# Optimization experiments

Hardware: AMD Instinct MI355X
Metric: run time of the kernel (lower is better)

The kernel has to match this reference:

```python
import jax, jax.numpy as jnp
import numpy as np


def _apply_ry(state, theta, i, n):
    # state: [B, 2^n] complex; theta: scalar or [B]
    B = state.shape[0]
    s = state.reshape(B, 2**i, 2, 2**(n - i - 1))
    th = jnp.reshape(theta, (-1, 1, 1)) * 0.5
    c, sn = jnp.cos(th), jnp.sin(th)
    a0, a1 = s[:, :, 0], s[:, :, 1]
    return jnp.stack([c * a0 - sn * a1, sn * a0 + c * a1], axis=2).reshape(B, -1)


def _apply_rz(state, theta, i, n):
    B = state.shape[0]
    s = state.reshape(B, 2**i, 2, 2**(n - i - 1))
    ph = jnp.exp(-0.5j * jnp.reshape(theta, (-1, 1, 1)).astype(jnp.float32))
    return jnp.stack([s[:, :, 0] * ph, s[:, :, 1] * jnp.conj(ph)], axis=2).reshape(B, -1)


def _apply_cnot(state, c, t, n):
    # CNOT(control=c, target=t); flips target amplitudes on control=1 slice
    B = state.shape[0]
    s = state.reshape((B,) + (2,) * n)
    ax_c, ax_t = 1 + c, 1 + t
    zero = jnp.take(s, 0, axis=ax_c)
    one = jnp.take(s, 1, axis=ax_c)
    one = jnp.flip(one, axis=ax_t - (1 if t > c else 0))
    return jnp.stack([zero, one], axis=ax_c).reshape(B, -1)


def _z_signs(n):
    # signs[i, k] = +1 if bit i of basis index k is 0 else -1 (qubit 0 = MSB)
    idx = np.arange(2**n)
    bits = (idx[None, :] >> (n - 1 - np.arange(n))[:, None]) & 1
    return jnp.asarray(1.0 - 2.0 * bits, dtype=jnp.float32)  # [n, 2^n]


def _circuit(q_in, w_ry, w_rz):
    # Batched state-vector simulation of: AngleEmbedding(RY) ->
    # n_layers x (per-qubit RY,RZ + CNOT ring) -> <Z_i> expectations.
    B, n = q_in.shape
    L = w_ry.shape[0]
    state = jnp.zeros((B, 2**n), jnp.complex64).at[:, 0].set(1.0)
    for i in range(n):  # AngleEmbedding with rotation='Y'
        state = _apply_ry(state, q_in[:, i], i, n)
    for l in range(L):
        for i in range(n):
            state = _apply_ry(state, w_ry[l, i], i, n)
            state = _apply_rz(state, w_rz[l, i], i, n)
        for i in range(n):  # CNOT ring
            state = _apply_cnot(state, i, (i + 1) % n, n)
    probs = jnp.abs(state) ** 2  # [B, 2^n]
    return probs @ _z_signs(n).T  # [B, n] = <Z_i>


def setup_inputs():
    key = jax.random.key(0)
    ks = jax.random.split(key, 6)
    B, D, n, L = 4096, 512, 10, 4
    return {
        "x": jax.random.normal(ks[0], (B, D), jnp.float32),
        "pre_w": jax.random.normal(ks[1], (n, D), jnp.float32) / np.sqrt(D).astype(np.float32),
        "pre_b": jnp.zeros((n,), jnp.float32),
        "post_w": jax.random.normal(ks[2], (1, n), jnp.float32) / np.sqrt(n).astype(np.float32),
        "post_b": jnp.zeros((1,), jnp.float32),
        "w_ry": jax.random.normal(ks[3], (L, n), jnp.float32),
        "w_rz": jax.random.normal(ks[4], (L, n), jnp.float32),
    }


def reference(x, pre_w, pre_b, post_w, post_b, w_ry, w_rz):
    q_in = x @ pre_w.T + pre_b      # pre_net: [B, n_qubits] rotation angles
    z = _circuit(q_in, w_ry, w_rz)  # [B, n_qubits] PauliZ expectations
    return z @ post_w.T + post_b    # post_net: [B, 1] logits
```

## Files before the change

### kernel.cpp

```cpp
#include <hip/hip_runtime.h>

#define DEV static __device__ __forceinline__

template <int CTRL>
DEV float dpp_mov(float v) {
    int i = __float_as_int(v);
    i = __builtin_amdgcn_update_dpp(i, i, CTRL, 0xF, 0xF, false);
    return __int_as_float(i);
}
template <int PAT>
DEV float swz(float v) {
    return __int_as_float(__builtin_amdgcn_ds_swizzle(__float_as_int(v), PAT));
}
DEV float bperm(int byteaddr, float v) {
    return __int_as_float(__builtin_amdgcn_ds_bpermute(byteaddr, __float_as_int(v)));
}

#if __has_builtin(__builtin_amdgcn_permlane16_swap)
#define HAVE_PL16 1
DEV void pl16_pair(float v, float &r0, float &r1) {
    auto r = __builtin_amdgcn_permlane16_swap(__float_as_int(v), __float_as_int(v),
                                              false, false);
    r0 = __int_as_float((int)r[0]);
    r1 = __int_as_float((int)r[1]);
}
#endif
#if __has_builtin(__builtin_amdgcn_permlane32_swap)
#define HAVE_PL32 1
DEV void pl32_pair(float v, float &r0, float &r1) {
    auto r = __builtin_amdgcn_permlane32_swap(__float_as_int(v), __float_as_int(v),
                                              false, false);
    r0 = __int_as_float((int)r[0]);
    r1 = __int_as_float((int)r[1]);
}
#endif

DEV float wave_sum(float v, int a32) {
    v += dpp_mov<0xB1>(v);
    v += dpp_mov<0x4E>(v);
    v += dpp_mov<0x141>(v);
    v += dpp_mov<0x128>(v);
#ifdef HAVE_PL16
    {
        float r0, r1;
        pl16_pair(v, r0, r1);
        v = r0 + r1;
    }
#else
    v += swz<0x401F>(v);
#endif
#ifdef HAVE_PL32
    {
        float r0, r1;
        pl32_pair(v, r0, r1);
        v = r0 + r1;
    }
#else
    v += bperm(a32, v);
#endif
    return v;
}

template <int P>
DEV void apply_ry(float (&re)[16], float (&im)[16], float c, float s, int lane,
                  int a32, bool cv16, bool cv32) {
    if constexpr (P == 9) {
#ifdef HAVE_PL32
        const bool hi = (lane & 32) != 0;
        const float fl = hi ? s : c;
        const float fh = hi ? c : -s;
        const float g0 = cv32 ? fl : fh;
        const float g1 = cv32 ? fh : fl;
#pragma unroll
        for (int r = 0; r < 16; ++r) {
            float x0, x1, y0, y1;
            pl32_pair(re[r], x0, x1);
            pl32_pair(im[r], y0, y1);
            re[r] = fmaf(g0, x0, g1 * x1);
            im[r] = fmaf(g0, y0, g1 * y1);
        }
#else
        const float sg = (lane & 32) ? s : -s;
#pragma unroll
        for (int r = 0; r < 16; ++r) {
            float pr = bperm(a32, re[r]);
            float pi = bperm(a32, im[r]);
            re[r] = fmaf(c, re[r], sg * pr);
            im[r] = fmaf(c, im[r], sg * pi);
        }
#endif
    } else if constexpr (P == 8) {
#ifdef HAVE_PL16
        const bool hi = (lane & 16) != 0;
        const float fl = hi ? s : c;
        const float fh = hi ? c : -s;
        const float g0 = cv16 ? fl : fh;
        const float g1 = cv16 ? fh : fl;
#pragma unroll
        for (int r = 0; r < 16; ++r) {
            float x0, x1, y0, y1;
            pl16_pair(re[r], x0, x1);
            pl16_pair(im[r], y0, y1);
            re[r] = fmaf(g0, x0, g1 * x1);
            im[r] = fmaf(g0, y0, g1 * y1);
        }
#else
        const float sg = (lane & 16) ? s : -s;
#pragma unroll
        for (int r = 0; r < 16; ++r) {
            float pr = swz<0x401F>(re[r]);
            float pi = swz<0x401F>(im[r]);
            re[r] = fmaf(c, re[r], sg * pr);
            im[r] = fmaf(c, im[r], sg * pi);
        }
#endif
    } else if constexpr (P >= 4) {
        constexpr int mask = 1 << (P - 4);
        const float sg = (lane & mask) ? s : -s;
#pragma unroll
        for (int r = 0; r < 16; ++r) {
            float pr, pi;
            if constexpr (mask == 8) {
                pr = dpp_mov<0x128>(re[r]);
                pi = dpp_mov<0x128>(im[r]);
            } else if constexpr (mask == 4) {
                pr = dpp_mov<0x1B>(dpp_mov<0x141>(re[r]));
                pi = dpp_mov<0x1B>(dpp_mov<0x141>(im[r]));
            } else if constexpr (mask == 2) {
                pr = dpp_mov<0x4E>(re[r]);
                pi = dpp_mov<0x4E>(im[r]);
            } else {
                pr = dpp_mov<0xB1>(re[r]);
                pi = dpp_mov<0xB1>(im[r]);
            }
            re[r] = fmaf(c, re[r], sg * pr);
            im[r] = fmaf(c, im[r], sg * pi);
        }
    } else {
        constexpr int tb = 1 << P;
#pragma unroll
        for (int r = 0; r < 16; ++r) {
            if (!(r & tb)) {
                const int r2 = r | tb;
                float a0r = re[r], a1r = re[r2];
                float a0i = im[r], a1i = im[r2];
                re[r]  = fmaf(c, a0r, -s * a1r);
                re[r2] = fmaf(s, a0r,  c * a1r);
                im[r]  = fmaf(c, a0i, -s * a1i);
                im[r2] = fmaf(s, a0i,  c * a1i);
            }
        }
    }
}

DEV int g_of(int a) {
    a ^= ((a >> 1) & 1) ? 1 : 0;
    a ^= ((a >> 2) & 1) ? 2 : 0;
    a ^= ((a >> 3) & 1) ? 4 : 0;
    a ^= ((a >> 4) & 1) ? 8 : 0;
    a ^= ((a >> 5) & 1) ? 16 : 0;
    return a;
}

__global__ __launch_bounds__(256, 4) void dqc_main_kernel(
    const float* __restrict__ x, const float* __restrict__ pre_w,
    const float* __restrict__ pre_b, const float* __restrict__ post_w,
    const float* __restrict__ post_b, const float* __restrict__ w_ry,
    const float* __restrict__ w_rz, float* __restrict__ out, int B) {
    const int lane = threadIdx.x & 63;
    const int wid = threadIdx.x >> 6;
    const int b = blockIdx.x * 4 + wid;
    if (b >= B) return;

    const int a32 = (lane ^ 32) << 2;

    bool cv16 = false, cv32 = false;
#ifdef HAVE_PL16
    {
        auto r = __builtin_amdgcn_permlane16_swap(lane, lane, false, false);
        cv16 = ((int)r[0] == (lane & ~16));
    }
#endif
#ifdef HAVE_PL32
    {
        auto r = __builtin_amdgcn_permlane32_swap(lane, lane, false, false);
        cv32 = ((int)r[0] == (lane & ~32));
    }
#endif

    const int h0 = lane ^ ((lane & 1) ? 32 : 0);
    const int cA = g_of(h0) << 2;
    const int cB = g_of(h0 ^ 32) << 2;

    float th[10];
#pragma unroll
    for (int i = 0; i < 10; ++i) th[i] = 0.f;
    const float4* xb4 = reinterpret_cast<const float4*>(x + (size_t)b * 512);
    const float4* pw4 = reinterpret_cast<const float4*>(pre_w);
#pragma unroll
    for (int k = 0; k < 2; ++k) {
        const int idx = lane + 64 * k;
        const float4 xv = xb4[idx];
#pragma unroll
        for (int i = 0; i < 10; ++i) {
            const float4 wv = pw4[i * 128 + idx];
            th[i] = fmaf(xv.x, wv.x, th[i]);
            th[i] = fmaf(xv.y, wv.y, th[i]);
            th[i] = fmaf(xv.z, wv.z, th[i]);
            th[i] = fmaf(xv.w, wv.w, th[i]);
        }
    }
#pragma unroll
    for (int i = 0; i < 10; ++i) th[i] = wave_sum(th[i], a32) + pre_b[i];

    float cc[10], ss[10];
#pragma unroll
    for (int i = 0; i < 10; ++i) {
        float a = th[i] * 0.5f;
        cc[i] = __cosf(a);
        ss[i] = __sinf(a);
    }
    float laneP = 1.f;
#pragma unroll
    for (int i = 0; i < 6; ++i)
        laneP *= ((lane >> (5 - i)) & 1) ? ss[i] : cc[i];
    float hi4[4], lo4[4];
#pragma unroll
    for (int j = 0; j < 4; ++j) {
        float f6 = (j >> 1) ? ss[6] : cc[6];
        float f7 = (j & 1) ? ss[7] : cc[7];
        hi4[j] = laneP * f6 * f7;
        float f8 = (j >> 1) ? ss[8] : cc[8];
        float f9 = (j & 1) ? ss[9] : cc[9];
        lo4[j] = f8 * f9;
    }
    float re[16], im[16];
#pragma unroll
    for (int r = 0; r < 16; ++r) { re[r] = hi4[r >> 2] * lo4[r & 3]; im[r] = 0.f; }

#pragma unroll 1
    for (int l = 0; l < 4; ++l) {
        const float* wry = w_ry + l * 10;
        const float* wrz = w_rz + l * 10;

        {
            float a;
            a = wry[0] * 0.5f; apply_ry<9>(re, im, __cosf(a), __sinf(a), lane, a32, cv16, cv32);
            a = wry[1] * 0.5f; apply_ry<8>(re, im, __cosf(a), __sinf(a), lane, a32, cv16, cv32);
            a = wry[2] * 0.5f; apply_ry<7>(re, im, __cosf(a), __sinf(a), lane, a32, cv16, cv32);
            a = wry[3] * 0.5f; apply_ry<6>(re, im, __cosf(a), __sinf(a), lane, a32, cv16, cv32);
            a = wry[4] * 0.5f; apply_ry<5>(re, im, __cosf(a), __sinf(a), lane, a32, cv16, cv32);
            a = wry[5] * 0.5f; apply_ry<4>(re, im, __cosf(a), __sinf(a), lane, a32, cv16, cv32);
            a = wry[6] * 0.5f; apply_ry<3>(re, im, __cosf(a), __sinf(a), lane, a32, cv16, cv32);
            a = wry[7] * 0.5f; apply_ry<2>(re, im, __cosf(a), __sinf(a), lane, a32, cv16, cv32);
            a = wry[8] * 0.5f; apply_ry<1>(re, im, __cosf(a), __sinf(a), lane, a32, cv16, cv32);
            a = wry[9] * 0.5f; apply_ry<0>(re, im, __cosf(a), __sinf(a), lane, a32, cv16, cv32);
        }

        float zc[10], zs[10];
#pragma unroll
        for (int q = 0; q < 10; ++q) {
            float a = wrz[q] * 0.5f;
            zc[q] = __cosf(a);
            zs[q] = __sinf(a);
        }
        float plr, pli;
        {
            pli = ((lane >> 5) & 1) ? zs[0] : -zs[0];
            plr = zc[0];
#pragma unroll
            for (int q = 1; q < 6; ++q) {
                float sq = ((lane >> (5 - q)) & 1) ? zs[q] : -zs[q];
                float nr = plr * zc[q] - pli * sq;
                float ni = plr * sq + pli * zc[q];
                plr = nr; pli = ni;
            }
        }
        float p67r[4], p67i[4], p89r[4], p89i[4];
        {
            const float c6 = zc[6], s6 = zs[6], c7 = zc[7], s7 = zs[7];
            const float c8 = zc[8], s8 = zs[8], c9 = zc[9], s9 = zs[9];
#pragma unroll
            for (int j = 0; j < 4; ++j) {
                float sg6 = (j >> 1) ? s6 : -s6;
                float sg7 = (j & 1) ? s7 : -s7;
                float ar = c6 * c7 - sg6 * sg7;
                float ai = c6 * sg7 + sg6 * c7;
                p67r[j] = ar * plr - ai * pli;
                p67i[j] = ar * pli + ai * plr;
                float sg8 = (j >> 1) ? s8 : -s8;
                float sg9 = (j & 1) ? s9 : -s9;
                p89r[j] = c8 * c9 - sg8 * sg9;
                p89i[j] = c8 * sg9 + sg8 * c9;
            }
        }
#pragma unroll
        for (int r = 0; r < 16; ++r) {
            const int j = r >> 2, k = r & 3;
            float t_r = re[r] * p67r[j] - im[r] * p67i[j];
            float t_i = re[r] * p67i[j] + im[r] * p67r[j];
            re[r] = t_r * p89r[k] - t_i * p89i[k];
            im[r] = t_r * p89i[k] + t_i * p89r[k];
        }

#pragma unroll
        for (int r = 0; r < 16; ++r) {
            const int addr = ((0x6996 >> r) & 1) ? cB : cA;
            re[r] = bperm(addr, re[r]);
            im[r] = bperm(addr, im[r]);
        }
        {
            const bool ctrl = (lane & 1) != 0;
#pragma unroll
            for (int r = 0; r < 8; ++r) {
                const int r2 = r | 8;
                float t0 = re[r], t1 = re[r2];
                re[r]  = ctrl ? t1 : t0;
                re[r2] = ctrl ? t0 : t1;
                float u0 = im[r], u1 = im[r2];
                im[r]  = ctrl ? u1 : u0;
                im[r2] = ctrl ? u0 : u1;
            }
        }
#pragma unroll
        for (int r = 0; r < 16; ++r)
            if ((r & 8) && !(r & 4)) {
                const int r2 = r | 4;
                float t = re[r]; re[r] = re[r2]; re[r2] = t;
                t = im[r]; im[r] = im[r2]; im[r2] = t;
            }
#pragma unroll
        for (int r = 0; r < 16; ++r)
            if ((r & 4) && !(r & 2)) {
                const int r2 = r | 2;
                float t = re[r]; re[r] = re[r2]; re[r2] = t;
                t = im[r]; im[r] = im[r2]; im[r2] = t;
            }
#pragma unroll
        for (int r = 0; r < 16; ++r)
            if ((r & 2) && !(r & 1)) {
                const int r2 = r | 1;
                float t = re[r]; re[r] = re[r2]; re[r2] = t;
                t = im[r]; im[r] = im[r2]; im[r2] = t;
            }
    }

    float laneC = 0.f;
#pragma unroll
    for (int j = 0; j < 6; ++j) {
        int bit = (lane >> (5 - j)) & 1;
        laneC += post_w[j] * (1.f - 2.f * (float)bit);
    }
    float acc = 0.f;
#pragma unroll
    for (int r = 0; r < 16; ++r) {
        float regC = 0.f;
#pragma unroll
        for (int j = 6; j < 10; ++j) {
            int bit = (r >> (9 - j)) & 1;
            regC += post_w[j] * (1.f - 2.f * (float)bit);
        }
        float p = fmaf(re[r], re[r], im[r] * im[r]);
        acc = fmaf(p, laneC + regC, acc);
    }
    acc = wave_sum(acc, a32);
    if (lane == 0) out[b] = acc + post_b[0];
}

extern "C" void kernel_launch(void* const* d_in, const int* in_sizes, int n_in,
                              void* d_out, int out_size, void* d_ws, size_t ws_size,
                              hipStream_t stream) {
    const float* x      = (const float*)d_in[0];
    const float* pre_w  = (const float*)d_in[1];
    const float* pre_b  = (const float*)d_in[2];
    const float* post_w = (const float*)d_in[3];
    const float* post_b = (const float*)d_in[4];
    const float* w_ry   = (const float*)d_in[5];
    const float* w_rz   = (const float*)d_in[6];
    float* out = (float*)d_out;
    (void)d_ws; (void)ws_size;

    const int B = in_sizes[0] / 512;

    dqc_main_kernel<<<(B + 3) / 4, 256, 0, stream>>>(x, pre_w, pre_b, post_w,
                                                     post_b, w_ry, w_rz, out, B);
}
```

Before: 106.5 us.

## Precompute layer trig in shared memory and peel real-only first layer

Each block now computes the sin/cos of all RY/RZ layer weights once into shared memory, so waves no longer evaluate the same transcendentals repeatedly. The first layer is peeled out: the state is purely real until the first RZ, so a real-only RY path halves the cross-lane shuffles and FMAs, and RZ is applied as a real-times-complex multiply. The final expectation weights are rebuilt from small lookup tables. This adds a __syncthreads and shared memory use, and the peeled layer grows code size and possibly register pressure.

```diff
diff --git a/kernel.cpp b/kernel.cpp
--- a/kernel.cpp
+++ b/kernel.cpp
@@ -60,6 +60,7 @@
 #endif
     return v;
 }
+
 
 template <int P>
 DEV void apply_ry(float (&re)[16], float (&im)[16], float c, float s, int lane,
@@ -153,6 +154,82 @@
     }
 }
 
+template <int P>
+DEV void apply_ry_real(float (&re)[16], float c, float s, int lane, int a32,
+                       bool cv16, bool cv32) {
+    if constexpr (P == 9) {
+#ifdef HAVE_PL32
+        const bool hi = (lane & 32) != 0;
+        const float fl = hi ? s : c;
+        const float fh = hi ? c : -s;
+        const float g0 = cv32 ? fl : fh;
+        const float g1 = cv32 ? fh : fl;
+#pragma unroll
+        for (int r = 0; r < 16; ++r) {
+            float x0, x1;
+            pl32_pair(re[r], x0, x1);
+            re[r] = fmaf(g0, x0, g1 * x1);
+        }
+#else
+        const float sg = (lane & 32) ? s : -s;
+#pragma unroll
+        for (int r = 0; r < 16; ++r) {
+            float pr = bperm(a32, re[r]);
+            re[r] = fmaf(c, re[r], sg * pr);
+        }
+#endif
+    } else if constexpr (P == 8) {
+#ifdef HAVE_PL16
+        const bool hi = (lane & 16) != 0;
+        const float fl = hi ? s : c;
+        const float fh = hi ? c : -s;
+        const float g0 = cv16 ? fl : fh;
+        const float g1 = cv16 ? fh : fl;
+#pragma unroll
+        for (int r = 0; r < 16; ++r) {
+            float x0, x1;
+            pl16_pair(re[r], x0, x1);
+            re[r] = fmaf(g0, x0, g1 * x1);
+        }
+#else
+        const float sg = (lane & 16) ? s : -s;
+#pragma unroll
+        for (int r = 0; r < 16; ++r) {
+            float pr = swz<0x401F>(re[r]);
+            re[r] = fmaf(c, re[r], sg * pr);
+        }
+#endif
+    } else if constexpr (P >= 4) {
+        constexpr int mask = 1 << (P - 4);
+        const float sg = (lane & mask) ? s : -s;
+#pragma unroll
+        for (int r = 0; r < 16; ++r) {
+            float pr;
+            if constexpr (mask == 8) {
+                pr = dpp_mov<0x128>(re[r]);
+            } else if constexpr (mask == 4) {
+                pr = dpp_mov<0x1B>(dpp_mov<0x141>(re[r]));
+            } else if constexpr (mask == 2) {
+                pr = dpp_mov<0x4E>(re[r]);
+            } else {
+                pr = dpp_mov<0xB1>(re[r]);
+            }
+            re[r] = fmaf(c, re[r], sg * pr);
+        }
+    } else {
+        constexpr int tb = 1 << P;
+#pragma unroll
+        for (int r = 0; r < 16; ++r) {
+            if (!(r & tb)) {
+                const int r2 = r | tb;
+                float a0 = re[r], a1 = re[r2];
+                re[r]  = fmaf(c, a0, -s * a1);
+                re[r2] = fmaf(s, a0,  c * a1);
+            }
+        }
+    }
+}
+
 DEV int g_of(int a) {
     a ^= ((a >> 1) & 1) ? 1 : 0;
     a ^= ((a >> 2) & 1) ? 2 : 0;
@@ -162,11 +239,96 @@
     return a;
 }
 
+DEV void build_rz_tables(const float (&zc)[10], const float (&zs)[10], int lane,
+                         float (&p67r)[4], float (&p67i)[4], float (&p89r)[4],
+                         float (&p89i)[4]) {
+    float plr, pli;
+    pli = ((lane >> 5) & 1) ? zs[0] : -zs[0];
+    plr = zc[0];
+#pragma unroll
+    for (int q = 1; q < 6; ++q) {
+        float sq = ((lane >> (5 - q)) & 1) ? zs[q] : -zs[q];
+        float nr = plr * zc[q] - pli * sq;
+        float ni = plr * sq + pli * zc[q];
+        plr = nr; pli = ni;
+    }
+    const float c6 = zc[6], s6 = zs[6], c7 = zc[7], s7 = zs[7];
+    const float c8 = zc[8], s8 = zs[8], c9 = zc[9], s9 = zs[9];
+#pragma unroll
+    for (int j = 0; j < 4; ++j) {
+        float sg6 = (j >> 1) ? s6 : -s6;
+        float sg7 = (j & 1) ? s7 : -s7;
+        float ar = c6 * c7 - sg6 * sg7;
+        float ai = c6 * sg7 + sg6 * c7;
+        p67r[j] = ar * plr - ai * pli;
+        p67i[j] = ar * pli + ai * plr;
+        float sg8 = (j >> 1) ? s8 : -s8;
+        float sg9 = (j & 1) ? s9 : -s9;
+        p89r[j] = c8 * c9 - sg8 * sg9;
+        p89i[j] = c8 * sg9 + sg8 * c9;
+    }
+}
+
+DEV void cnot_ring(float (&re)[16], float (&im)[16], int cA, int cB, int lane) {
+#pragma unroll
+    for (int r = 0; r < 16; ++r) {
+        const int addr = ((0x6996 >> r) & 1) ? cB : cA;
+        re[r] = bperm(addr, re[r]);
+        im[r] = bperm(addr, im[r]);
+    }
+    {
+        const bool ctrl = (lane & 1) != 0;
+#pragma unroll
+        for (int r = 0; r < 8; ++r) {
+            const int r2 = r | 8;
+            float t0 = re[r], t1 = re[r2];
+            re[r]  = ctrl ? t1 : t0;
+            re[r2] = ctrl ? t0 : t1;
+            float u0 = im[r], u1 = im[r2];
+            im[r]  = ctrl ? u1 : u0;
+            im[r2] = ctrl ? u0 : u1;
+        }
+    }
+#pragma unroll
+    for (int r = 0; r < 16; ++r)
+        if ((r & 8) && !(r & 4)) {
+            const int r2 = r | 4;
+            float t = re[r]; re[r] = re[r2]; re[r2] = t;
+            t = im[r]; im[r] = im[r2]; im[r2] = t;
+        }
+#pragma unroll
+    for (int r = 0; r < 16; ++r)
+        if ((r & 4) && !(r & 2)) {
+            const int r2 = r | 2;
+            float t = re[r]; re[r] = re[r2]; re[r2] = t;
+            t = im[r]; im[r] = im[r2]; im[r2] = t;
+        }
+#pragma unroll
+    for (int r = 0; r < 16; ++r)
+        if ((r & 2) && !(r & 1)) {
+            const int r2 = r | 1;
+            float t = re[r]; re[r] = re[r2]; re[r2] = t;
+            t = im[r]; im[r] = im[r2]; im[r2] = t;
+        }
+}
+
 __global__ __launch_bounds__(256, 4) void dqc_main_kernel(
     const float* __restrict__ x, const float* __restrict__ pre_w,
     const float* __restrict__ pre_b, const float* __restrict__ post_w,
     const float* __restrict__ post_b, const float* __restrict__ w_ry,
     const float* __restrict__ w_rz, float* __restrict__ out, int B) {
+    __shared__ float2 sh_trig[80];
+    {
+        int t = threadIdx.x;
+        if (t < 80) {
+            float ang = (t < 40 ? w_ry[t] : w_rz[t - 40]) * 0.5f;
+            float sv, cv;
+            __sincosf(ang, &sv, &cv);
+            sh_trig[t] = make_float2(cv, sv);
+        }
+    }
+    __syncthreads();
+
     const int lane = threadIdx.x & 63;
     const int wid = threadIdx.x >> 6;
     const int b = blockIdx.x * 4 + wid;
@@ -216,9 +378,10 @@
     float cc[10], ss[10];
 #pragma unroll
     for (int i = 0; i < 10; ++i) {
-        float a = th[i] * 0.5f;
-        cc[i] = __cosf(a);
-        ss[i] = __sinf(a);
+        float sv, cv;
+        __sincosf(th[i] * 0.5f, &sv, &cv);
+        cc[i] = cv;
+        ss[i] = sv;
     }
     float laneP = 1.f;
 #pragma unroll
@@ -236,64 +399,69 @@
     }
     float re[16], im[16];
 #pragma unroll
-    for (int r = 0; r < 16; ++r) { re[r] = hi4[r >> 2] * lo4[r & 3]; im[r] = 0.f; }
+    for (int r = 0; r < 16; ++r) re[r] = hi4[r >> 2] * lo4[r & 3];
+
+    {
+        float yc[10], ys[10];
+#pragma unroll
+        for (int q = 0; q < 10; ++q) {
+            float2 v = sh_trig[q];
+            yc[q] = v.x; ys[q] = v.y;
+        }
+        apply_ry_real<9>(re, yc[0], ys[0], lane, a32, cv16, cv32);
+        apply_ry_real<8>(re, yc[1], ys[1], lane, a32, cv16, cv32);
+        apply_ry_real<7>(re, yc[2], ys[2], lane, a32, cv16, cv32);
+        apply_ry_real<6>(re, yc[3], ys[3], lane, a32, cv16, cv32);
+        apply_ry_real<5>(re, yc[4], ys[4], lane, a32, cv16, cv32);
+        apply_ry_real<4>(re, yc[5], ys[5], lane, a32, cv16, cv32);
+        apply_ry_real<3>(re, yc[6], ys[6], lane, a32, cv16, cv32);
+        apply_ry_real<2>(re, yc[7], ys[7], lane, a32, cv16, cv32);
+        apply_ry_real<1>(re, yc[8], ys[8], lane, a32, cv16, cv32);
+        apply_ry_real<0>(re, yc[9], ys[9], lane, a32, cv16, cv32);
+
+        float zc[10], zs[10];
+#pragma unroll
+        for (int q = 0; q < 10; ++q) {
+            float2 v = sh_trig[40 + q];
+            zc[q] = v.x; zs[q] = v.y;
+        }
+        float p67r[4], p67i[4], p89r[4], p89i[4];
+        build_rz_tables(zc, zs, lane, p67r, p67i, p89r, p89i);
+#pragma unroll
+        for (int r = 0; r < 16; ++r) {
+            const int j = r >> 2, k = r & 3;
+            float Ar = p67r[j] * p89r[k] - p67i[j] * p89i[k];
+            float Ai = p67r[j] * p89i[k] + p67i[j] * p89r[k];
+            float t = re[r];
+            re[r] = t * Ar;
+            im[r] = t * Ai;
+        }
+        cnot_ring(re, im, cA, cB, lane);
+    }
 
 #pragma unroll 1
-    for (int l = 0; l < 4; ++l) {
-        const float* wry = w_ry + l * 10;
-        const float* wrz = w_rz + l * 10;
-
-        {
-            float a;
-            a = wry[0] * 0.5f; apply_ry<9>(re, im, __cosf(a), __sinf(a), lane, a32, cv16, cv32);
-            a = wry[1] * 0.5f; apply_ry<8>(re, im, __cosf(a), __sinf(a), lane, a32, cv16, cv32);
-            a = wry[2] * 0.5f; apply_ry<7>(re, im, __cosf(a), __sinf(a), lane, a32, cv16, cv32);
-            a = wry[3] * 0.5f; apply_ry<6>(re, im, __cosf(a), __sinf(a), lane, a32, cv16, cv32);
-            a = wry[4] * 0.5f; apply_ry<5>(re, im, __cosf(a), __sinf(a), lane, a32, cv16, cv32);
-            a = wry[5] * 0.5f; apply_ry<4>(re, im, __cosf(a), __sinf(a), lane, a32, cv16, cv32);
-            a = wry[6] * 0.5f; apply_ry<3>(re, im, __cosf(a), __sinf(a), lane, a32, cv16, cv32);
-            a = wry[7] * 0.5f; apply_ry<2>(re, im, __cosf(a), __sinf(a), lane, a32, cv16, cv32);
-            a = wry[8] * 0.5f; apply_ry<1>(re, im, __cosf(a), __sinf(a), lane, a32, cv16, cv32);
-            a = wry[9] * 0.5f; apply_ry<0>(re, im, __cosf(a), __sinf(a), lane, a32, cv16, cv32);
-        }
-
-        float zc[10], zs[10];
+    for (int l = 1; l < 4; ++l) {
+        float yc[10], ys[10], zc[10], zs[10];
 #pragma unroll
         for (int q = 0; q < 10; ++q) {
-            float a = wrz[q] * 0.5f;
-            zc[q] = __cosf(a);
-            zs[q] = __sinf(a);
-        }
-        float plr, pli;
-        {
-            pli = ((lane >> 5) & 1) ? zs[0] : -zs[0];
-            plr = zc[0];
-#pragma unroll
-            for (int q = 1; q < 6; ++q) {
-                float sq = ((lane >> (5 - q)) & 1) ? zs[q] : -zs[q];
-                float nr = plr * zc[q] - pli * sq;
-                float ni = plr * sq + pli * zc[q];
-                plr = nr; pli = ni;
-            }
-        }
+            float2 v = sh_trig[l * 10 + q];
+            yc[q] = v.x; ys[q] = v.y;
+            float2 w = sh_trig[40 + l * 10 + q];
+            zc[q] = w.x; zs[q] = w.y;
+        }
+        apply_ry<9>(re, im, yc[0], ys[0], lane, a32, cv16, cv32);
+        apply_ry<8>(re, im, yc[1], ys[1], lane, a32, cv16, cv32);
+        apply_ry<7>(re, im, yc[2], ys[2], lane, a32, cv16, cv32);
+        apply_ry<6>(re, im, yc[3], ys[3], lane, a32, cv16, cv32);
+        apply_ry<5>(re, im, yc[4], ys[4], lane, a32, cv16, cv32);
+        apply_ry<4>(re, im, yc[5], ys[5], lane, a32, cv16, cv32);
+        apply_ry<3>(re, im, yc[6], ys[6], lane, a32, cv16, cv32);
+        apply_ry<2>(re, im, yc[7], ys[7], lane, a32, cv16, cv32);
+        apply_ry<1>(re, im, yc[8], ys[8], lane, a32, cv16, cv32);
+        apply_ry<0>(re, im, yc[9], ys[9], lane, a32, cv16, cv32);
+
         float p67r[4], p67i[4], p89r[4], p89i[4];
-        {
-            const float c6 = zc[6], s6 = zs[6], c7 = zc[7], s7 = zs[7];
-            const float c8 = zc[8], s8 = zs[8], c9 = zc[9], s9 = zs[9];
-#pragma unroll
-            for (int j = 0; j < 4; ++j) {
-                float sg6 = (j >> 1) ? s6 : -s6;
-                float sg7 = (j & 1) ? s7 : -s7;
-                float ar = c6 * c7 - sg6 * sg7;
-                float ai = c6 * sg7 + sg6 * c7;
-                p67r[j] = ar * plr - ai * pli;
-                p67i[j] = ar * pli + ai * plr;
-                float sg8 = (j >> 1) ? s8 : -s8;
-                float sg9 = (j & 1) ? s9 : -s9;
-                p89r[j] = c8 * c9 - sg8 * sg9;
-                p89i[j] = c8 * sg9 + sg8 * c9;
-            }
-        }
+        build_rz_tables(zc, zs, lane, p67r, p67i, p89r, p89i);
 #pragma unroll
         for (int r = 0; r < 16; ++r) {
             const int j = r >> 2, k = r & 3;
@@ -302,47 +470,7 @@
             re[r] = t_r * p89r[k] - t_i * p89i[k];
             im[r] = t_r * p89i[k] + t_i * p89r[k];
         }
-
-#pragma unroll
-        for (int r = 0; r < 16; ++r) {
-            const int addr = ((0x6996 >> r) & 1) ? cB : cA;
-            re[r] = bperm(addr, re[r]);
-            im[r] = bperm(addr, im[r]);
-        }
-        {
-            const bool ctrl = (lane & 1) != 0;
-#pragma unroll
-            for (int r = 0; r < 8; ++r) {
-                const int r2 = r | 8;
-                float t0 = re[r], t1 = re[r2];
-                re[r]  = ctrl ? t1 : t0;
-                re[r2] = ctrl ? t0 : t1;
-                float u0 = im[r], u1 = im[r2];
-                im[r]  = ctrl ? u1 : u0;
-                im[r2] = ctrl ? u0 : u1;
-            }
-        }
-#pragma unroll
-        for (int r = 0; r < 16; ++r)
-            if ((r & 8) && !(r & 4)) {
-                const int r2 = r | 4;
-                float t = re[r]; re[r] = re[r2]; re[r2] = t;
-                t = im[r]; im[r] = im[r2]; im[r2] = t;
-            }
-#pragma unroll
-        for (int r = 0; r < 16; ++r)
-            if ((r & 4) && !(r & 2)) {
-                const int r2 = r | 2;
-                float t = re[r]; re[r] = re[r2]; re[r2] = t;
-                t = im[r]; im[r] = im[r2]; im[r2] = t;
-            }
-#pragma unroll
-        for (int r = 0; r < 16; ++r)
-            if ((r & 2) && !(r & 1)) {
-                const int r2 = r | 1;
-                float t = re[r]; re[r] = re[r2]; re[r2] = t;
-                t = im[r]; im[r] = im[r2]; im[r2] = t;
-            }
+        cnot_ring(re, im, cA, cB, lane);
     }
 
     float laneC = 0.f;
@@ -351,17 +479,18 @@
         int bit = (lane >> (5 - j)) & 1;
         laneC += post_w[j] * (1.f - 2.f * (float)bit);
     }
+    const float w6 = post_w[6], w7 = post_w[7], w8 = post_w[8], w9 = post_w[9];
+    float base67[4], m89[4];
+#pragma unroll
+    for (int j = 0; j < 4; ++j) {
+        base67[j] = laneC + ((j >> 1) ? -w6 : w6) + ((j & 1) ? -w7 : w7);
+        m89[j] = ((j >> 1) ? -w8 : w8) + ((j & 1) ? -w9 : w9);
+    }
     float acc = 0.f;
 #pragma unroll
     for (int r = 0; r < 16; ++r) {
-        float regC = 0.f;
-#pragma unroll
-        for (int j = 6; j < 10; ++j) {
-            int bit = (r >> (9 - j)) & 1;
-            regC += post_w[j] * (1.f - 2.f * (float)bit);
-        }
         float p = fmaf(re[r], re[r], im[r] * im[r]);
-        acc = fmaf(p, laneC + regC, acc);
+        acc = fmaf(p, base67[r >> 2] + m89[r & 3], acc);
     }
     acc = wave_sum(acc, a32);
     if (lane == 0) out[b] = acc + post_b[0];
```

Result: faster. 99.22 us (-6.8%).

## Fold first-layer rotations into product-state init and cache gate trig in LDS

Applied to the files above, without the earlier changes.

The embedding RY and the first layer's RY (same axis) are merged by adding their angles, and with the first RZ layer this gives a product state built analytically per lane. That removes one full layer of RY butterflies and one RZ pass, and the remaining three layers are fully unrolled. Per-gate sin/cos are computed once per block into shared memory instead of per wave. Smaller tweaks swap a double-DPP shuffle for one ds_swizzle and precompute the post-net sign weights. In exchange the kernel gains a block barrier and a larger unrolled body that may raise register pressure.

```diff
diff --git a/kernel.cpp b/kernel.cpp
--- a/kernel.cpp
+++ b/kernel.cpp
@@ -124,8 +124,8 @@
                 pr = dpp_mov<0x128>(re[r]);
                 pi = dpp_mov<0x128>(im[r]);
             } else if constexpr (mask == 4) {
-                pr = dpp_mov<0x1B>(dpp_mov<0x141>(re[r]));
-                pi = dpp_mov<0x1B>(dpp_mov<0x141>(im[r]));
+                pr = swz<0x101F>(re[r]);
+                pi = swz<0x101F>(im[r]);
             } else if constexpr (mask == 2) {
                 pr = dpp_mov<0x4E>(re[r]);
                 pi = dpp_mov<0x4E>(im[r]);
@@ -162,11 +162,96 @@
     return a;
 }
 
+DEV void build_rz_tables(const float (&zc)[10], const float (&zs)[10], int lane,
+                         float (&p67r)[4], float (&p67i)[4], float (&p89r)[4],
+                         float (&p89i)[4]) {
+    float plr, pli;
+    pli = ((lane >> 5) & 1) ? zs[0] : -zs[0];
+    plr = zc[0];
+#pragma unroll
+    for (int q = 1; q < 6; ++q) {
+        float sq = ((lane >> (5 - q)) & 1) ? zs[q] : -zs[q];
+        float nr = plr * zc[q] - pli * sq;
+        float ni = plr * sq + pli * zc[q];
+        plr = nr; pli = ni;
+    }
+    const float c6 = zc[6], s6 = zs[6], c7 = zc[7], s7 = zs[7];
+    const float c8 = zc[8], s8 = zs[8], c9 = zc[9], s9 = zs[9];
+#pragma unroll
+    for (int j = 0; j < 4; ++j) {
+        float sg6 = (j >> 1) ? s6 : -s6;
+        float sg7 = (j & 1) ? s7 : -s7;
+        float ar = c6 * c7 - sg6 * sg7;
+        float ai = c6 * sg7 + sg6 * c7;
+        p67r[j] = ar * plr - ai * pli;
+        p67i[j] = ar * pli + ai * plr;
+        float sg8 = (j >> 1) ? s8 : -s8;
+        float sg9 = (j & 1) ? s9 : -s9;
+        p89r[j] = c8 * c9 - sg8 * sg9;
+        p89i[j] = c8 * sg9 + sg8 * c9;
+    }
+}
+
+DEV void cnot_ring(float (&re)[16], float (&im)[16], int cA, int cB, int lane) {
+#pragma unroll
+    for (int r = 0; r < 16; ++r) {
+        const int addr = ((0x6996 >> r) & 1) ? cB : cA;
+        re[r] = bperm(addr, re[r]);
+        im[r] = bperm(addr, im[r]);
+    }
+    {
+        const bool ctrl = (lane & 1) != 0;
+#pragma unroll
+        for (int r = 0; r < 8; ++r) {
+            const int r2 = r | 8;
+            float t0 = re[r], t1 = re[r2];
+            re[r]  = ctrl ? t1 : t0;
+            re[r2] = ctrl ? t0 : t1;
+            float u0 = im[r], u1 = im[r2];
+            im[r]  = ctrl ? u1 : u0;
+            im[r2] = ctrl ? u0 : u1;
+        }
+    }
+#pragma unroll
+    for (int r = 0; r < 16; ++r)
+        if ((r & 8) && !(r & 4)) {
+            const int r2 = r | 4;
+            float t = re[r]; re[r] = re[r2]; re[r2] = t;
+            t = im[r]; im[r] = im[r2]; im[r2] = t;
+        }
+#pragma unroll
+    for (int r = 0; r < 16; ++r)
+        if ((r & 4) && !(r & 2)) {
+            const int r2 = r | 2;
+            float t = re[r]; re[r] = re[r2]; re[r2] = t;
+            t = im[r]; im[r] = im[r2]; im[r2] = t;
+        }
+#pragma unroll
+    for (int r = 0; r < 16; ++r)
+        if ((r & 2) && !(r & 1)) {
+            const int r2 = r | 1;
+            float t = re[r]; re[r] = re[r2]; re[r2] = t;
+            t = im[r]; im[r] = im[r2]; im[r2] = t;
+        }
+}
+
 __global__ __launch_bounds__(256, 4) void dqc_main_kernel(
     const float* __restrict__ x, const float* __restrict__ pre_w,
     const float* __restrict__ pre_b, const float* __restrict__ post_w,
     const float* __restrict__ post_b, const float* __restrict__ w_ry,
     const float* __restrict__ w_rz, float* __restrict__ out, int B) {
+    __shared__ float2 sh_trig[80];
+    {
+        int t = threadIdx.x;
+        if (t < 80) {
+            float ang = (t < 40 ? w_ry[t] : w_rz[t - 40]) * 0.5f;
+            float sv, cv;
+            __sincosf(ang, &sv, &cv);
+            sh_trig[t] = make_float2(cv, sv);
+        }
+    }
+    __syncthreads();
+
     const int lane = threadIdx.x & 63;
     const int wid = threadIdx.x >> 6;
     const int b = blockIdx.x * 4 + wid;
@@ -213,87 +298,81 @@
 #pragma unroll
     for (int i = 0; i < 10; ++i) th[i] = wave_sum(th[i], a32) + pre_b[i];
 
-    float cc[10], ss[10];
-#pragma unroll
-    for (int i = 0; i < 10; ++i) {
-        float a = th[i] * 0.5f;
-        cc[i] = __cosf(a);
-        ss[i] = __sinf(a);
-    }
-    float laneP = 1.f;
-#pragma unroll
-    for (int i = 0; i < 6; ++i)
-        laneP *= ((lane >> (5 - i)) & 1) ? ss[i] : cc[i];
-    float hi4[4], lo4[4];
+    float f0r[10], f0i[10], f1r[10], f1i[10];
+#pragma unroll
+    for (int q = 0; q < 10; ++q) {
+        float hh = 0.5f * (th[q] + w_ry[q]);
+        float sh_, ch_;
+        __sincosf(hh, &sh_, &ch_);
+        float2 z = sh_trig[40 + q];
+        f0r[q] = ch_ * z.x;  f0i[q] = -ch_ * z.y;
+        f1r[q] = sh_ * z.x;  f1i[q] =  sh_ * z.y;
+    }
+    float Lr, Li;
+    {
+        int bq = (lane >> 5) & 1;
+        Lr = bq ? f1r[0] : f0r[0];
+        Li = bq ? f1i[0] : f0i[0];
+#pragma unroll
+        for (int q = 1; q < 6; ++q) {
+            int bb = (lane >> (5 - q)) & 1;
+            float br = bb ? f1r[q] : f0r[q];
+            float bi = bb ? f1i[q] : f0i[q];
+            float nr = Lr * br - Li * bi;
+            float ni = Lr * bi + Li * br;
+            Lr = nr; Li = ni;
+        }
+    }
+    float t67r[4], t67i[4], t89r[4], t89i[4];
 #pragma unroll
     for (int j = 0; j < 4; ++j) {
-        float f6 = (j >> 1) ? ss[6] : cc[6];
-        float f7 = (j & 1) ? ss[7] : cc[7];
-        hi4[j] = laneP * f6 * f7;
-        float f8 = (j >> 1) ? ss[8] : cc[8];
-        float f9 = (j & 1) ? ss[9] : cc[9];
-        lo4[j] = f8 * f9;
+        float ar = (j >> 1) ? f1r[6] : f0r[6];
+        float ai = (j >> 1) ? f1i[6] : f0i[6];
+        float br = (j & 1) ? f1r[7] : f0r[7];
+        float bi = (j & 1) ? f1i[7] : f0i[7];
+        float pr = ar * br - ai * bi;
+        float pi = ar * bi + ai * br;
+        t67r[j] = pr * Lr - pi * Li;
+        t67i[j] = pr * Li + pi * Lr;
+        float cr_ = (j >> 1) ? f1r[8] : f0r[8];
+        float ci_ = (j >> 1) ? f1i[8] : f0i[8];
+        float dr = (j & 1) ? f1r[9] : f0r[9];
+        float di = (j & 1) ? f1i[9] : f0i[9];
+        t89r[j] = cr_ * dr - ci_ * di;
+        t89i[j] = cr_ * di + ci_ * dr;
     }
     float re[16], im[16];
 #pragma unroll
-    for (int r = 0; r < 16; ++r) { re[r] = hi4[r >> 2] * lo4[r & 3]; im[r] = 0.f; }
-
-#pragma unroll 1
-    for (int l = 0; l < 4; ++l) {
-        const float* wry = w_ry + l * 10;
-        const float* wrz = w_rz + l * 10;
-
-        {
-            float a;
-            a = wry[0] * 0.5f; apply_ry<9>(re, im, __cosf(a), __sinf(a), lane, a32, cv16, cv32);
-            a = wry[1] * 0.5f; apply_ry<8>(re, im, __cosf(a), __sinf(a), lane, a32, cv16, cv32);
-            a = wry[2] * 0.5f; apply_ry<7>(re, im, __cosf(a), __sinf(a), lane, a32, cv16, cv32);
-            a = wry[3] * 0.5f; apply_ry<6>(re, im, __cosf(a), __sinf(a), lane, a32, cv16, cv32);
-            a = wry[4] * 0.5f; apply_ry<5>(re, im, __cosf(a), __sinf(a), lane, a32, cv16, cv32);
-            a = wry[5] * 0.5f; apply_ry<4>(re, im, __cosf(a), __sinf(a), lane, a32, cv16, cv32);
-            a = wry[6] * 0.5f; apply_ry<3>(re, im, __cosf(a), __sinf(a), lane, a32, cv16, cv32);
-            a = wry[7] * 0.5f; apply_ry<2>(re, im, __cosf(a), __sinf(a), lane, a32, cv16, cv32);
-            a = wry[8] * 0.5f; apply_ry<1>(re, im, __cosf(a), __sinf(a), lane, a32, cv16, cv32);
-            a = wry[9] * 0.5f; apply_ry<0>(re, im, __cosf(a), __sinf(a), lane, a32, cv16, cv32);
-        }
-
-        float zc[10], zs[10];
+    for (int r = 0; r < 16; ++r) {
+        const int j = r >> 2, k = r & 3;
+        re[r] = t67r[j] * t89r[k] - t67i[j] * t89i[k];
+        im[r] = t67r[j] * t89i[k] + t67i[j] * t89r[k];
+    }
+    cnot_ring(re, im, cA, cB, lane);
+
+#pragma unroll
+    for (int l = 1; l < 4; ++l) {
+        float yc[10], ys[10], zc[10], zs[10];
 #pragma unroll
         for (int q = 0; q < 10; ++q) {
-            float a = wrz[q] * 0.5f;
-            zc[q] = __cosf(a);
-            zs[q] = __sinf(a);
-        }
-        float plr, pli;
-        {
-            pli = ((lane >> 5) & 1) ? zs[0] : -zs[0];
-            plr = zc[0];
-#pragma unroll
-            for (int q = 1; q < 6; ++q) {
-                float sq = ((lane >> (5 - q)) & 1) ? zs[q] : -zs[q];
-                float nr = plr * zc[q] - pli * sq;
-                float ni = plr * sq + pli * zc[q];
-                plr = nr; pli = ni;
-            }
-        }
+            float2 v = sh_trig[l * 10 + q];
+            yc[q] = v.x; ys[q] = v.y;
+            float2 w = sh_trig[40 + l * 10 + q];
+            zc[q] = w.x; zs[q] = w.y;
+        }
+        apply_ry<9>(re, im, yc[0], ys[0], lane, a32, cv16, cv32);
+        apply_ry<8>(re, im, yc[1], ys[1], lane, a32, cv16, cv32);
+        apply_ry<7>(re, im, yc[2], ys[2], lane, a32, cv16, cv32);
+        apply_ry<6>(re, im, yc[3], ys[3], lane, a32, cv16, cv32);
+        apply_ry<5>(re, im, yc[4], ys[4], lane, a32, cv16, cv32);
+        apply_ry<4>(re, im, yc[5], ys[5], lane, a32, cv16, cv32);
+        apply_ry<3>(re, im, yc[6], ys[6], lane, a32, cv16, cv32);
+        apply_ry<2>(re, im, yc[7], ys[7], lane, a32, cv16, cv32);
+        apply_ry<1>(re, im, yc[8], ys[8], lane, a32, cv16, cv32);
+        apply_ry<0>(re, im, yc[9], ys[9], lane, a32, cv16, cv32);
+
         float p67r[4], p67i[4], p89r[4], p89i[4];
-        {
-            const float c6 = zc[6], s6 = zs[6], c7 = zc[7], s7 = zs[7];
-            const float c8 = zc[8], s8 = zs[8], c9 = zc[9], s9 = zs[9];
-#pragma unroll
-            for (int j = 0; j < 4; ++j) {
-                float sg6 = (j >> 1) ? s6 : -s6;
-                float sg7 = (j & 1) ? s7 : -s7;
-                float ar = c6 * c7 - sg6 * sg7;
-                float ai = c6 * sg7 + sg6 * c7;
-                p67r[j] = ar * plr - ai * pli;
-                p67i[j] = ar * pli + ai * plr;
-                float sg8 = (j >> 1) ? s8 : -s8;
-                float sg9 = (j & 1) ? s9 : -s9;
-                p89r[j] = c8 * c9 - sg8 * sg9;
-                p89i[j] = c8 * sg9 + sg8 * c9;
-            }
-        }
+        build_rz_tables(zc, zs, lane, p67r, p67i, p89r, p89i);
 #pragma unroll
         for (int r = 0; r < 16; ++r) {
             const int j = r >> 2, k = r & 3;
@@ -302,47 +381,7 @@
             re[r] = t_r * p89r[k] - t_i * p89i[k];
             im[r] = t_r * p89i[k] + t_i * p89r[k];
         }
-
-#pragma unroll
-        for (int r = 0; r < 16; ++r) {
-            const int addr = ((0x6996 >> r) & 1) ? cB : cA;
-            re[r] = bperm(addr, re[r]);
-            im[r] = bperm(addr, im[r]);
-        }
-        {
-            const bool ctrl = (lane & 1) != 0;
-#pragma unroll
-            for (int r = 0; r < 8; ++r) {
-                const int r2 = r | 8;
-                float t0 = re[r], t1 = re[r2];
-                re[r]  = ctrl ? t1 : t0;
-                re[r2] = ctrl ? t0 : t1;
-                float u0 = im[r], u1 = im[r2];
-                im[r]  = ctrl ? u1 : u0;
-                im[r2] = ctrl ? u0 : u1;
-            }
-        }
-#pragma unroll
-        for (int r = 0; r < 16; ++r)
-            if ((r & 8) && !(r & 4)) {
-                const int r2 = r | 4;
-                float t = re[r]; re[r] = re[r2]; re[r2] = t;
-                t = im[r]; im[r] = im[r2]; im[r2] = t;
-            }
-#pragma unroll
-        for (int r = 0; r < 16; ++r)
-            if ((r & 4) && !(r & 2)) {
-                const int r2 = r | 2;
-                float t = re[r]; re[r] = re[r2]; re[r2] = t;
-                t = im[r]; im[r] = im[r2]; im[r2] = t;
-            }
-#pragma unroll
-        for (int r = 0; r < 16; ++r)
-            if ((r & 2) && !(r & 1)) {
-                const int r2 = r | 1;
-                float t = re[r]; re[r] = re[r2]; re[r2] = t;
-                t = im[r]; im[r] = im[r2]; im[r2] = t;
-            }
+        cnot_ring(re, im, cA, cB, lane);
     }
 
     float laneC = 0.f;
@@ -351,17 +390,18 @@
         int bit = (lane >> (5 - j)) & 1;
         laneC += post_w[j] * (1.f - 2.f * (float)bit);
     }
+    const float w6 = post_w[6], w7 = post_w[7], w8 = post_w[8], w9 = post_w[9];
+    float base67[4], m89[4];
+#pragma unroll
+    for (int j = 0; j < 4; ++j) {
+        base67[j] = laneC + ((j >> 1) ? -w6 : w6) + ((j & 1) ? -w7 : w7);
+        m89[j] = ((j >> 1) ? -w8 : w8) + ((j & 1) ? -w9 : w9);
+    }
     float acc = 0.f;
 #pragma unroll
     for (int r = 0; r < 16; ++r) {
-        float regC = 0.f;
-#pragma unroll
-        for (int j = 6; j < 10; ++j) {
-            int bit = (r >> (9 - j)) & 1;
-            regC += post_w[j] * (1.f - 2.f * (float)bit);
-        }
         float p = fmaf(re[r], re[r], im[r] * im[r]);
-        acc = fmaf(p, laneC + regC, acc);
+        acc = fmaf(p, base67[r >> 2] + m89[r & 3], acc);
     }
     acc = wave_sum(acc, a32);
     if (lane == 0) out[b] = acc + post_b[0];
```

Result: faster. 95.82 us (-10.0%).
